# Performance work log

Hardware: AMD Instinct MI355X
Metric: run time of the kernel (lower is better)

Reference implementation:

```python
import jax, jax.numpy as jnp
import numpy as np

HO, WO = 64, 64
SHARPNESS = 150.0


def _stereographic_grid(ho, wo):
    # Matches create_normal_grid(..., 'stereographic'); torch.meshgrid 'ij':
    # v varies over rows (ho), u over cols (wo).
    v, u = np.meshgrid(np.arange(ho), np.arange(wo), indexing='ij')
    p = 4.0 * ((u + 0.5) / wo - 0.5)
    q = -4.0 * ((v + 0.5) / ho - 0.5)
    d = 1.0 + p ** 2 + q ** 2
    z = -(-1.0 + p ** 2 + q ** 2) / d
    m = (z > 0.0).astype(np.float32)
    x = 2.0 * p / d * m
    y = 2.0 * q / d * m
    z = z * m
    return np.stack([x, y, z], axis=-1).reshape(-1, 3).astype(np.float32)  # [ho*wo,3]


_GRID = _stereographic_grid(HO, WO)
_IDX = np.nonzero(np.any(_GRID != 0, axis=-1))[0]  # static valid-query indices [N]
_QN = _GRID[_IDX]  # [N,3]


def setup_inputs() -> dict:
    key = jax.random.key(0)
    k1, k2, k3 = jax.random.split(key, 3)
    bs, c, h, w = 2, 64, 192, 192
    in_fea_map = jax.random.normal(k1, (bs, c, h, w), dtype=jnp.float32)
    nrm = jax.random.normal(k2, (bs, 3, h, w), dtype=jnp.float32)
    in_normal_map = nrm / (jnp.linalg.norm(nrm, axis=1, keepdims=True) + 1e-8)
    in_mask_map = (jax.random.uniform(k3, (bs, 1, h, w)) > 0.2).astype(jnp.float32)
    log_query_norm = jnp.full((1,), np.log(SHARPNESS), dtype=jnp.float32)
    return {"in_fea_map": in_fea_map, "in_normal_map": in_normal_map,
            "in_mask_map": in_mask_map, "log_query_norm": log_query_norm}


def reference(in_fea_map, in_normal_map, in_mask_map, log_query_norm):
    bs, c, h, w = in_fea_map.shape
    hw = h * w
    qn = jnp.asarray(_QN, dtype=in_fea_map.dtype)  # [N,3] static valid queries
    vals = in_fea_map.reshape(bs, c, hw).transpose(0, 2, 1)       # [bs,HW,c]
    key_n = in_normal_map.reshape(bs, 3, hw)                       # [bs,3,HW]
    cos = jnp.einsum('nd,bdm->bnm', qn, key_n)                     # [bs,N,HW]
    dps = cos / np.float32(np.sqrt(3.0))
    dps = dps - jnp.max(dps, axis=-1, keepdims=True)
    w_ = jnp.exp(jnp.exp(log_query_norm) * dps)                    # dropout in eval = identity
    w_ = w_ * in_mask_map.reshape(bs, 1, hw)
    weights = w_ / (jnp.sum(w_, axis=-1, keepdims=True) + 1e-9)    # [bs,N,HW]
    mapped = weights @ vals                                        # [bs,N,c]
    mapped = jnp.concatenate([jnp.broadcast_to(qn, (bs,) + qn.shape), mapped], axis=-1)
    # variance map over last 3 feature channels
    mean = mapped[..., -3:]
    sq_mean = weights @ (vals[..., -3:] ** 2)
    var = jnp.sum(sq_mean - mean ** 2, axis=-1, keepdims=True)
    mapped = jnp.concatenate([var, mapped], axis=-1)
    # cosine map
    rm_cos = jnp.sum(weights * cos, axis=-1, keepdims=True)
    mapped = jnp.concatenate([rm_cos, mapped], axis=-1)            # [bs,N,c+5]
    C = mapped.shape[-1]
    out = jnp.zeros((bs, HO * WO, C), mapped.dtype).at[:, _IDX, :].set(mapped)
    return out.transpose(0, 2, 1).reshape(bs, C, HO, WO)
```

## Files before the change

### kernel.cpp

```cpp
#include <hip/hip_runtime.h>
#include <hip/hip_bf16.h>
#include <cstdint>
#include <cstddef>

#define HW 36864
#define QT 64
#define NCHA 69

constexpr bool is_valid_px(int v, int u) {
  int a = 2 * u - 63, b = 2 * v - 63;
  return a * a + b * b < 1024;
}
constexpr int count_valid() {
  int n = 0;
  for (int v = 0; v < 64; ++v)
    for (int u = 0; u < 64; ++u)
      if (is_valid_px(v, u)) ++n;
  return n;
}
constexpr int NV  = count_valid();
constexpr int NQT = (NV + QT - 1) / QT;
constexpr int NQP = NQT * QT;
constexpr int PLANE = 2 * NQP * NCHA;

struct QTab {
  short idx[NQP];
  short rank[4096];
};
constexpr QTab make_qtab() {
  QTab t{};
  int n = 0;
  for (int p = 0; p < 4096; ++p) {
    int v = p >> 6, u = p & 63;
    if (is_valid_px(v, u)) { t.idx[n] = (short)p; t.rank[p] = (short)n; ++n; }
    else t.rank[p] = -1;
  }
  for (int i = n; i < NQP; ++i) t.idx[i] = -1;
  return t;
}
__constant__ QTab g_qtab = make_qtab();

typedef short short8 __attribute__((ext_vector_type(8)));
typedef float f32x4  __attribute__((ext_vector_type(4)));

__device__ __forceinline__ unsigned short f2b(float f) {
  unsigned int u = __float_as_uint(f);
  u += 0x7FFFu + ((u >> 16) & 1u);
  return (unsigned short)(u >> 16);
}
__device__ __forceinline__ ushort2 f2b2(float a, float b) {
  __hip_bfloat162 h = __float22bfloat162_rn(make_float2(a, b));
  return *(ushort2*)&h;
}
__device__ __forceinline__ ushort4 f2b4(float4 v) {
  ushort4 r;
  *(ushort2*)&r.x = f2b2(v.x, v.y);
  *(ushort2*)&r.z = f2b2(v.z, v.w);
  return r;
}
__device__ __forceinline__ void pix2qn(int pix, float& x, float& y, float& z) {
  x = 0.f; y = 0.f; z = 0.f;
  if (pix >= 0) {
    int v = pix >> 6, u = pix & 63;
    float p = (float)(2 * u - 63) * (1.0f / 32.0f);
    float q = -(float)(2 * v - 63) * (1.0f / 32.0f);
    float d = 1.0f + p * p + q * q;
    x = 2.0f * p / d; y = 2.0f * q / d; z = (1.0f - p * p - q * q) / d;
  }
}


template<int KSC>
__global__ __launch_bounds__(256) void partial_kernel(
    const float* __restrict__ fea,
    const float* __restrict__ nrm,
    const float* __restrict__ msk,
    const float* __restrict__ lqn,
    float* __restrict__ part)
{
  constexpr int SLICE  = HW / KSC;
  constexpr int NCHUNK = SLICE / 64;

  __shared__ __align__(16) unsigned short v_s[2][80][72];
  __shared__ __align__(16) float nrm4_s[2][64][4];
  __shared__ float ex_s[64][9];

  const int bx  = blockIdx.x;
  const int cls = bx & 7;
  const int r0  = bx >> 3;
  const int qt  = r0 % NQT;
  const int sh  = r0 / NQT;
  const int s   = sh * 8 + cls;
  const int b   = s / KSC;
  const int ks  = s % KSC;

  const int t    = threadIdx.x;
  const int wv   = t >> 6;
  const int l    = t & 63;
  const int lq   = l >> 4;
  const int mrow = l & 15;

  const float Cc = __expf(lqn[0]) * 0.57735026919f;

  float qx, qy, qz;
  pix2qn(g_qtab.idx[qt * QT + 16 * wv + mrow], qx, qy, qz);

  if (t < 160) {
    int row = 70 + (t >> 4);
    int p4  = (t & 15) * 4;
    unsigned short c = (row == 70) ? (unsigned short)0x3F80 : (unsigned short)0;
    ushort4 cv; cv.x = c; cv.y = c; cv.z = c; cv.w = c;
    *(ushort4*)&v_s[0][row][p4] = cv;
    *(ushort4*)&v_s[1][row][p4] = cv;
  }

  const size_t base_f = (size_t)b * 64 * HW;
  const size_t base_n = (size_t)b * 3 * HW;
  const size_t base_m = (size_t)b * HW;

  const int chb = t >> 4;
  const int px4 = (t & 15) * 4;
  const int arr = t >> 6;
  const int pxp = 32 * (l >> 5) + 4 * (l & 7) + ((l >> 3) & 3);

  f32x4 acc[5];
  #pragma unroll
  for (int nt = 0; nt < 5; ++nt) acc[nt] = (f32x4)(0.0f);

  float4 pf[4];
  float pn = 0.f, pm = 0.f;

  auto load_chunk = [&](int ck) {
    int m0 = ks * SLICE + ck * 64;
    #pragma unroll
    for (int i = 0; i < 4; ++i)
      pf[i] = *(const float4*)(fea + base_f + (size_t)(chb + 16 * i) * HW + (size_t)(m0 + px4));
    if (arr < 3) pn = nrm[base_n + (size_t)arr * HW + (size_t)(m0 + l)];
    else         pm = msk[base_m + (size_t)(m0 + l)];
  };
  auto store_chunk = [&](int buf) {
    #pragma unroll
    for (int i = 0; i < 4; ++i) {
      int ch = chb + 16 * i;
      float4 fv = pf[i];
      *(ushort4*)&v_s[buf][ch][px4] = f2b4(fv);
      if (ch >= 61) {
        float4 sq = make_float4(fv.x * fv.x, fv.y * fv.y, fv.z * fv.z, fv.w * fv.w);
        *(ushort4*)&v_s[buf][ch + 3][px4] = f2b4(sq);
      }
    }
    if (arr < 3) {
      v_s[buf][67 + arr][l] = f2b(pn);
      nrm4_s[buf][pxp][arr] = Cc * pn;
    } else {
      nrm4_s[buf][pxp][3] = -Cc + (pm > 0.5f ? 0.f : -2000.f);
    }
  };

  load_chunk(0);
  store_chunk(0);
  __syncthreads();

  for (int ck = 0; ck < NCHUNK; ++ck) {
    const int buf = ck & 1;
    if (ck + 1 < NCHUNK) load_chunk(ck + 1);

    #pragma unroll
    for (int kk = 0; kk < 64; kk += 32) {
      float e[8];
      #pragma unroll
      for (int j = 0; j < 8; ++j) {
        const float4 nv = *(const float4*)&nrm4_s[buf][kk + 4 * j + lq][0];
        float tt = fmaf(qx, nv.x, fmaf(qy, nv.y, fmaf(qz, nv.z, nv.w)));
        e[j] = __expf(tt);
      }
      short8 a;
      #pragma unroll
      for (int p = 0; p < 4; ++p) {
        ushort2 pr = f2b2(e[2 * p], e[2 * p + 1]);
        a[2 * p]     = (short)pr.x;
        a[2 * p + 1] = (short)pr.y;
      }
      #pragma unroll
      for (int nt = 0; nt < 5; ++nt) {
        short8 bb = *(const short8*)&v_s[buf][16 * nt + mrow][kk + 8 * lq];
        acc[nt] = __builtin_amdgcn_mfma_f32_16x16x32_bf16(a, bb, acc[nt], 0, 0, 0);
      }
    }

    if (ck + 1 < NCHUNK) {
      store_chunk(buf ^ 1);
      __syncthreads();
    }
  }

  const size_t pbase = (size_t)ks * PLANE + ((size_t)b * NQP + (size_t)(qt * QT)) * NCHA;
  #pragma unroll
  for (int nt = 0; nt < 4; ++nt) {
    #pragma unroll
    for (int rr = 0; rr < 4; ++rr) {
      int qloc = 16 * wv + 4 * lq + rr;
      part[pbase + (size_t)qloc * NCHA + (size_t)(16 * nt + mrow)] = acc[nt][rr];
    }
  }
  if (mrow < 7) {
    #pragma unroll
    for (int rr = 0; rr < 4; ++rr)
      ex_s[16 * wv + 4 * lq + rr][mrow] = acc[4][rr];
  }
  __syncthreads();
  if (t < 64) {
    float gx, gy, gz;
    pix2qn(g_qtab.idx[qt * QT + t], gx, gy, gz);
    float swc = gx * ex_s[t][3] + gy * ex_s[t][4] + gz * ex_s[t][5];
    size_t o = pbase + (size_t)t * NCHA;
    part[o + 64] = ex_s[t][0];
    part[o + 65] = ex_s[t][1];
    part[o + 66] = ex_s[t][2];
    part[o + 67] = swc;
    part[o + 68] = ex_s[t][6];
  }
}

#define NFIN (2 * NQT * 4)
#define NTAIL 256

__global__ __launch_bounds__(256) void finalize_kernel(
    const float* __restrict__ part,
    float* __restrict__ out,
    int ksc)
{
  const int blk = blockIdx.x;
  const int t   = threadIdx.x;

  if (blk < NFIN) {
    __shared__ float sm[16][NCHA];
    const int b   = blk / (NQT * 4);
    const int rem = blk % (NQT * 4);
    const int qt  = rem >> 2;
    const int qr  = rem & 3;
    const int q0  = qt * QT + qr * 16;

    const size_t colbase = ((size_t)b * NQP + (size_t)q0) * NCHA;
    for (int i = t; i < 16 * NCHA; i += 256) {
      float sv = 0.f;
      const size_t off = colbase + (size_t)i;
      #pragma unroll 8
      for (int k = 0; k < ksc; ++k) sv += part[(size_t)k * PLANE + off];
      sm[0][i] = sv;
    }
    __syncthreads();

    for (int i = t; i < 16 * NCHA; i += 256) {
      const int ql = i / NCHA;
      const int oc = i % NCHA;
      const int pix = g_qtab.idx[q0 + ql];
      if (pix < 0) continue;
      const float* A = sm[ql];
      const float inv = 1.0f / (A[68] + 1e-9f);
      float gx, gy, gz;
      pix2qn(pix, gx, gy, gz);
      float val;
      if (oc == 0)      val = A[67] * inv;
      else if (oc == 1) {
        val = 0.f;
        #pragma unroll
        for (int j = 0; j < 3; ++j) {
          float m  = A[61 + j] * inv;
          float sq = A[64 + j] * inv;
          val += sq - m * m;
        }
      }
      else if (oc == 2) val = gx;
      else if (oc == 3) val = gy;
      else if (oc == 4) val = gz;
      else              val = A[oc - 5] * inv;
      out[((size_t)b * NCHA + (size_t)oc) * 4096 + pix] = val;
    }
  } else {
    const int start = (blk - NFIN) * 256 + t;
    const int strd  = (NTAIL - NFIN) * 256;
    const int TOT   = 2 * NCHA * 4096;
    for (int i = start; i < TOT; i += strd) {
      if (g_qtab.rank[i & 4095] < 0) out[i] = 0.0f;
    }
  }
}

extern "C" void kernel_launch(void* const* d_in, const int* in_sizes, int n_in,
                              void* d_out, int out_size, void* d_ws, size_t ws_size,
                              hipStream_t stream) {
  const float* fea = (const float*)d_in[0];
  const float* nrm = (const float*)d_in[1];
  const float* msk = (const float*)d_in[2];
  const float* lqn = (const float*)d_in[3];
  float* part = (float*)d_ws;
  float* out  = (float*)d_out;

  const size_t need32 = (size_t)PLANE * 32 * sizeof(float);
  if (ws_size >= need32) {
    partial_kernel<32><<<dim3(2 * 32 * NQT), 256, 0, stream>>>(fea, nrm, msk, lqn, part);
    finalize_kernel<<<dim3(NTAIL), 256, 0, stream>>>(part, out, 32);
  } else {
    partial_kernel<16><<<dim3(2 * 16 * NQT), 256, 0, stream>>>(fea, nrm, msk, lqn, part);
    finalize_kernel<<<dim3(NTAIL), 256, 0, stream>>>(part, out, 16);
  }
}
```

Before: 122.0 us.

## Halve partial-kernel block to two waves, each computing two 16-query tiles

The partial kernel now runs 128 threads (2 waves) per block instead of 256, and each wave computes two 16-query MFMA tiles that share the same LDS B-operand loads. Each thread loads twice as many feature rows per chunk. The finalize kernel is split into more, smaller blocks of 8 queries. This reuses each B fragment across two MFMAs and lowers the per-block thread count, but doubles the accumulator registers and exp work per thread.

```diff
diff --git a/kernel.cpp b/kernel.cpp
--- a/kernel.cpp
+++ b/kernel.cpp
@@ -71,7 +71,7 @@
 
 
 template<int KSC>
-__global__ __launch_bounds__(256) void partial_kernel(
+__global__ __launch_bounds__(128, 2) void partial_kernel(
     const float* __restrict__ fea,
     const float* __restrict__ nrm,
     const float* __restrict__ msk,
@@ -102,12 +102,13 @@
 
   const float Cc = __expf(lqn[0]) * 0.57735026919f;
 
-  float qx, qy, qz;
-  pix2qn(g_qtab.idx[qt * QT + 16 * wv + mrow], qx, qy, qz);
-
-  if (t < 160) {
-    int row = 70 + (t >> 4);
-    int p4  = (t & 15) * 4;
+  float qx[2], qy[2], qz[2];
+  pix2qn(g_qtab.idx[qt * QT + 32 * wv + mrow],      qx[0], qy[0], qz[0]);
+  pix2qn(g_qtab.idx[qt * QT + 32 * wv + 16 + mrow], qx[1], qy[1], qz[1]);
+
+  for (int s0 = t; s0 < 160; s0 += 128) {
+    int row = 70 + (s0 >> 4);
+    int p4  = (s0 & 15) * 4;
     unsigned short c = (row == 70) ? (unsigned short)0x3F80 : (unsigned short)0;
     ushort4 cv; cv.x = c; cv.y = c; cv.z = c; cv.w = c;
     *(ushort4*)&v_s[0][row][p4] = cv;
@@ -120,28 +121,30 @@
 
   const int chb = t >> 4;
   const int px4 = (t & 15) * 4;
-  const int arr = t >> 6;
   const int pxp = 32 * (l >> 5) + 4 * (l & 7) + ((l >> 3) & 3);
 
-  f32x4 acc[5];
+  f32x4 acc[2][5];
   #pragma unroll
-  for (int nt = 0; nt < 5; ++nt) acc[nt] = (f32x4)(0.0f);
-
-  float4 pf[4];
-  float pn = 0.f, pm = 0.f;
+  for (int h = 0; h < 2; ++h)
+    #pragma unroll
+    for (int nt = 0; nt < 5; ++nt) acc[h][nt] = (f32x4)(0.0f);
+
+  float4 pf[8];
+  float pnA = 0.f, pnB = 0.f;
 
   auto load_chunk = [&](int ck) {
     int m0 = ks * SLICE + ck * 64;
     #pragma unroll
-    for (int i = 0; i < 4; ++i)
-      pf[i] = *(const float4*)(fea + base_f + (size_t)(chb + 16 * i) * HW + (size_t)(m0 + px4));
-    if (arr < 3) pn = nrm[base_n + (size_t)arr * HW + (size_t)(m0 + l)];
-    else         pm = msk[base_m + (size_t)(m0 + l)];
+    for (int i = 0; i < 8; ++i)
+      pf[i] = *(const float4*)(fea + base_f + (size_t)(chb + 8 * i) * HW + (size_t)(m0 + px4));
+    pnA = nrm[base_n + (size_t)wv * HW + (size_t)(m0 + l)];
+    pnB = (wv == 0) ? nrm[base_n + (size_t)2 * HW + (size_t)(m0 + l)]
+                    : msk[base_m + (size_t)(m0 + l)];
   };
   auto store_chunk = [&](int buf) {
     #pragma unroll
-    for (int i = 0; i < 4; ++i) {
-      int ch = chb + 16 * i;
+    for (int i = 0; i < 8; ++i) {
+      int ch = chb + 8 * i;
       float4 fv = pf[i];
       *(ushort4*)&v_s[buf][ch][px4] = f2b4(fv);
       if (ch >= 61) {
@@ -149,11 +152,13 @@
         *(ushort4*)&v_s[buf][ch + 3][px4] = f2b4(sq);
       }
     }
-    if (arr < 3) {
-      v_s[buf][67 + arr][l] = f2b(pn);
-      nrm4_s[buf][pxp][arr] = Cc * pn;
+    v_s[buf][67 + wv][l] = f2b(pnA);
+    nrm4_s[buf][pxp][wv] = Cc * pnA;
+    if (wv == 0) {
+      v_s[buf][69][l] = f2b(pnB);
+      nrm4_s[buf][pxp][2] = Cc * pnB;
     } else {
-      nrm4_s[buf][pxp][3] = -Cc + (pm > 0.5f ? 0.f : -2000.f);
+      nrm4_s[buf][pxp][3] = -Cc + (pnB > 0.5f ? 0.f : -2000.f);
     }
   };
 
@@ -167,24 +172,28 @@
 
     #pragma unroll
     for (int kk = 0; kk < 64; kk += 32) {
-      float e[8];
+      float e0[8], e1[8];
       #pragma unroll
       for (int j = 0; j < 8; ++j) {
         const float4 nv = *(const float4*)&nrm4_s[buf][kk + 4 * j + lq][0];
-        float tt = fmaf(qx, nv.x, fmaf(qy, nv.y, fmaf(qz, nv.z, nv.w)));
-        e[j] = __expf(tt);
-      }
-      short8 a;
+        float t0 = fmaf(qx[0], nv.x, fmaf(qy[0], nv.y, fmaf(qz[0], nv.z, nv.w)));
+        float t1 = fmaf(qx[1], nv.x, fmaf(qy[1], nv.y, fmaf(qz[1], nv.z, nv.w)));
+        e0[j] = __expf(t0);
+        e1[j] = __expf(t1);
+      }
+      short8 a0, a1;
       #pragma unroll
       for (int p = 0; p < 4; ++p) {
-        ushort2 pr = f2b2(e[2 * p], e[2 * p + 1]);
-        a[2 * p]     = (short)pr.x;
-        a[2 * p + 1] = (short)pr.y;
+        ushort2 p0 = f2b2(e0[2 * p], e0[2 * p + 1]);
+        ushort2 p1 = f2b2(e1[2 * p], e1[2 * p + 1]);
+        a0[2 * p] = (short)p0.x; a0[2 * p + 1] = (short)p0.y;
+        a1[2 * p] = (short)p1.x; a1[2 * p + 1] = (short)p1.y;
       }
       #pragma unroll
       for (int nt = 0; nt < 5; ++nt) {
         short8 bb = *(const short8*)&v_s[buf][16 * nt + mrow][kk + 8 * lq];
-        acc[nt] = __builtin_amdgcn_mfma_f32_16x16x32_bf16(a, bb, acc[nt], 0, 0, 0);
+        acc[0][nt] = __builtin_amdgcn_mfma_f32_16x16x32_bf16(a0, bb, acc[0][nt], 0, 0, 0);
+        acc[1][nt] = __builtin_amdgcn_mfma_f32_16x16x32_bf16(a1, bb, acc[1][nt], 0, 0, 0);
       }
     }
 
@@ -196,17 +205,20 @@
 
   const size_t pbase = (size_t)ks * PLANE + ((size_t)b * NQP + (size_t)(qt * QT)) * NCHA;
   #pragma unroll
-  for (int nt = 0; nt < 4; ++nt) {
-    #pragma unroll
-    for (int rr = 0; rr < 4; ++rr) {
-      int qloc = 16 * wv + 4 * lq + rr;
-      part[pbase + (size_t)qloc * NCHA + (size_t)(16 * nt + mrow)] = acc[nt][rr];
-    }
-  }
-  if (mrow < 7) {
-    #pragma unroll
-    for (int rr = 0; rr < 4; ++rr)
-      ex_s[16 * wv + 4 * lq + rr][mrow] = acc[4][rr];
+  for (int h = 0; h < 2; ++h) {
+    #pragma unroll
+    for (int nt = 0; nt < 4; ++nt) {
+      #pragma unroll
+      for (int rr = 0; rr < 4; ++rr) {
+        int qloc = 32 * wv + 16 * h + 4 * lq + rr;
+        part[pbase + (size_t)qloc * NCHA + (size_t)(16 * nt + mrow)] = acc[h][nt][rr];
+      }
+    }
+    if (mrow < 7) {
+      #pragma unroll
+      for (int rr = 0; rr < 4; ++rr)
+        ex_s[32 * wv + 16 * h + 4 * lq + rr][mrow] = acc[h][4][rr];
+    }
   }
   __syncthreads();
   if (t < 64) {
@@ -222,8 +234,8 @@
   }
 }
 
-#define NFIN (2 * NQT * 4)
-#define NTAIL 256
+#define NFIN (2 * NQT * 8)
+#define NTAIL (2 * NFIN)
 
 __global__ __launch_bounds__(256) void finalize_kernel(
     const float* __restrict__ part,
@@ -234,15 +246,15 @@
   const int t   = threadIdx.x;
 
   if (blk < NFIN) {
-    __shared__ float sm[16][NCHA];
-    const int b   = blk / (NQT * 4);
-    const int rem = blk % (NQT * 4);
-    const int qt  = rem >> 2;
-    const int qr  = rem & 3;
-    const int q0  = qt * QT + qr * 16;
+    __shared__ float sm[8][NCHA];
+    const int b   = blk / (NQT * 8);
+    const int rem = blk % (NQT * 8);
+    const int qt  = rem >> 3;
+    const int qr  = rem & 7;
+    const int q0  = qt * QT + qr * 8;
 
     const size_t colbase = ((size_t)b * NQP + (size_t)q0) * NCHA;
-    for (int i = t; i < 16 * NCHA; i += 256) {
+    for (int i = t; i < 8 * NCHA; i += 256) {
       float sv = 0.f;
       const size_t off = colbase + (size_t)i;
       #pragma unroll 8
@@ -251,7 +263,7 @@
     }
     __syncthreads();
 
-    for (int i = t; i < 16 * NCHA; i += 256) {
+    for (int i = t; i < 8 * NCHA; i += 256) {
       const int ql = i / NCHA;
       const int oc = i % NCHA;
       const int pix = g_qtab.idx[q0 + ql];
@@ -299,10 +311,10 @@
 
   const size_t need32 = (size_t)PLANE * 32 * sizeof(float);
   if (ws_size >= need32) {
-    partial_kernel<32><<<dim3(2 * 32 * NQT), 256, 0, stream>>>(fea, nrm, msk, lqn, part);
+    partial_kernel<32><<<dim3(2 * 32 * NQT), 128, 0, stream>>>(fea, nrm, msk, lqn, part);
     finalize_kernel<<<dim3(NTAIL), 256, 0, stream>>>(part, out, 32);
   } else {
-    partial_kernel<16><<<dim3(2 * 16 * NQT), 256, 0, stream>>>(fea, nrm, msk, lqn, part);
+    partial_kernel<16><<<dim3(2 * 16 * NQT), 128, 0, stream>>>(fea, nrm, msk, lqn, part);
     finalize_kernel<<<dim3(NTAIL), 256, 0, stream>>>(part, out, 16);
   }
 }
```

Result: no change. 121.2 us (-0.7%).
